# Kernel optimization log

Measured on AMD Instinct MI355X. Metric: run time of the kernel, lower is better.

The kernel has to match this reference:

```python
import jax, jax.numpy as jnp
import numpy as np

NEG_SLOPE = 0.2  # PyG GATv2Conv default negative_slope


def setup_inputs() -> dict:
    key = jax.random.key(0)
    ks = jax.random.split(key, 8)
    B, N, C, H, F, E = 16, 5000, 128, 2, 64, 1_280_000
    T = B * N
    s = 0.05
    x = jax.random.normal(ks[0], (B, N, C), jnp.float32)
    edge_index = jax.random.randint(ks[1], (2, E), 0, T, jnp.int32)
    Wl = jax.random.normal(ks[2], (C, H * F), jnp.float32) * s
    bl = jnp.zeros((H * F,), jnp.float32)
    Wr = jax.random.normal(ks[3], (C, H * F), jnp.float32) * s
    br = jnp.zeros((H * F,), jnp.float32)
    att = jax.random.normal(ks[4], (H, F), jnp.float32) * s
    bias = jnp.zeros((H * F,), jnp.float32)
    return {"x": x, "edge_index": edge_index, "Wl": Wl, "bl": bl,
            "Wr": Wr, "br": br, "att": att, "bias": bias}


def reference(x, edge_index, Wl, bl, Wr, br, att, bias):
    # x: (B, N, C) -> flatten to (T, C), T = B*N total nodes
    B, N, C = x.shape
    T = B * N
    H, F = att.shape
    xf = x.reshape(T, C)
    x_l = (xf @ Wl + bl).reshape(T, H, F)  # source transform (lin_l)
    x_r = (xf @ Wr + br).reshape(T, H, F)  # target transform (lin_r)
    # add self loops (add_self_loops=True)
    loops = jnp.arange(T, dtype=edge_index.dtype)
    src = jnp.concatenate([edge_index[0], loops])
    dst = jnp.concatenate([edge_index[1], loops])
    # GATv2 score: att . LeakyReLU(x_j + x_i)
    e = jax.nn.leaky_relu(x_l[src] + x_r[dst], NEG_SLOPE)  # (Et, H, F)
    logits = jnp.einsum('ehf,hf->eh', e, att)              # (Et, H)
    # edge softmax over incoming edges of each dst node
    m = jax.lax.stop_gradient(jax.ops.segment_max(logits, dst, num_segments=T))
    p = jnp.exp(logits - m[dst])
    denom = jax.ops.segment_sum(p, dst, num_segments=T)
    alpha = p / denom[dst]                                  # (Et, H)
    # aggregate: out_i = sum_j alpha_ij * x_l[j]
    out = jax.ops.segment_sum(x_l[src] * alpha[:, :, None], dst, num_segments=T)
    out = out.reshape(T, H * F) + bias  # concat=True -> (T, H*F)
    return out.reshape(B, N, H * F)
```

## Files before the change

### kernel.cpp

```cpp
#include <hip/hip_runtime.h>
#include <hip/hip_bf16.h>

typedef __hip_bfloat16 bf16;
typedef short s16x8 __attribute__((ext_vector_type(8)));
typedef float f32x4 __attribute__((ext_vector_type(4)));

#define NEG_SLOPE 0.2f
#define MAXB 160
#define EPB  4096
#define CAP  12288

__device__ __forceinline__ unsigned int f32_to_bf16_bits(float f) {
    unsigned int u = __float_as_uint(f);
    return (u + 0x7FFFu + ((u >> 16) & 1u)) >> 16;
}
__device__ __forceinline__ float bf16lo_to_f32(unsigned int u) {
    return __uint_as_float(u << 16);
}
__device__ __forceinline__ float bf16hi_to_f32(unsigned int u) {
    return __uint_as_float(u & 0xFFFF0000u);
}
__device__ __forceinline__ float loadf_rt(const void* p, size_t i, int isb) {
    return isb ? __bfloat162float(((const bf16*)p)[i]) : ((const float*)p)[i];
}

#define ROR_ADD(v, n)                                                          \
    v += __int_as_float(__builtin_amdgcn_update_dpp(                           \
        0, __float_as_int(v), 0x120 + (n), 0xF, 0xF, true))

__global__ void detect_dtype(const unsigned short* __restrict__ xh, int* __restrict__ flag)
{
    int lane = threadIdx.x;
    int cnt = 0;
    for (int j = lane; j < 256; j += 64) {
        unsigned short h = xh[j];
        int e = (h >> 7) & 0xFF;
        if ((h & 0x7FFF) == 0 || (e >= 117 && e <= 131)) cnt++;
    }
    #pragma unroll
    for (int off = 32; off; off >>= 1) cnt += __shfl_xor(cnt, off, 64);
    if (lane == 0) *flag = (cnt >= 192) ? 1 : 0;
}

__global__ void prep_w(const void* __restrict__ Wl, const void* __restrict__ Wr,
                       unsigned short* __restrict__ bpack, const int* __restrict__ flag)
{
    int isb = *flag;
    int tid = blockIdx.x * blockDim.x + threadIdx.x;
    if (tid >= 2 * 8 * 4 * 64) return;
    int lane = tid & 63;
    int kc   = (tid >> 6) & 3;
    int nt   = (tid >> 8) & 7;
    int mat  = tid >> 11;
    const void* W = mat ? Wr : Wl;
    int n  = nt * 16 + (lane & 15);
    int k0 = kc * 32 + (lane >> 4) * 8;
    unsigned short* o = bpack + (size_t)tid * 8;
    #pragma unroll
    for (int j = 0; j < 8; ++j)
        o[j] = (unsigned short)f32_to_bf16_bits(loadf_rt(W, (size_t)(k0 + j) * 128 + n, isb));
}

__global__ void gemm_mfma(const void* __restrict__ x,
                          const unsigned short* __restrict__ bpack,
                          const void* __restrict__ bl, const void* __restrict__ br,
                          unsigned int* __restrict__ xlp, unsigned int* __restrict__ xrp,
                          int T, const int* __restrict__ flag)
{
    int isb  = *flag;
    int lane = threadIdx.x & 63;
    int w    = blockIdx.x * 4 + (threadIdx.x >> 6);
    int row0 = w * 16;
    if (row0 >= T) return;
    int m = lane & 15, quad = lane >> 4;
    int arow = min(row0 + m, T - 1);

    f32x4 acc[16];
    #pragma unroll
    for (int nt = 0; nt < 16; ++nt) acc[nt] = (f32x4){0.f, 0.f, 0.f, 0.f};

    const s16x8* bp = (const s16x8*)bpack;
    for (int kc = 0; kc < 4; ++kc) {
        s16x8 a;
        if (isb) {
            const unsigned short* xb = (const unsigned short*)x
                                     + (size_t)arow * 128 + kc * 32 + quad * 8;
            a = *(const s16x8*)xb;
        } else {
            const float* xp = (const float*)x + (size_t)arow * 128 + kc * 32 + quad * 8;
            float4 xa = ((const float4*)xp)[0];
            float4 xc = ((const float4*)xp)[1];
            a[0] = (short)f32_to_bf16_bits(xa.x); a[1] = (short)f32_to_bf16_bits(xa.y);
            a[2] = (short)f32_to_bf16_bits(xa.z); a[3] = (short)f32_to_bf16_bits(xa.w);
            a[4] = (short)f32_to_bf16_bits(xc.x); a[5] = (short)f32_to_bf16_bits(xc.y);
            a[6] = (short)f32_to_bf16_bits(xc.z); a[7] = (short)f32_to_bf16_bits(xc.w);
        }
        #pragma unroll
        for (int nt = 0; nt < 16; ++nt) {
            s16x8 b = bp[(size_t)(((nt >> 3) * 32) + (nt & 7) * 4 + kc) * 64 + lane];
            acc[nt] = __builtin_amdgcn_mfma_f32_16x16x32_bf16(a, b, acc[nt], 0, 0, 0);
        }
    }
    #pragma unroll
    for (int nt = 0; nt < 4; ++nt) {
        int fl = nt * 16 + m;
        float bl0 = loadf_rt(bl, fl, isb), bl1 = loadf_rt(bl, 64 + fl, isb);
        float br0 = loadf_rt(br, fl, isb), br1 = loadf_rt(br, 64 + fl, isb);
        #pragma unroll
        for (int r = 0; r < 4; ++r) {
            int t = row0 + quad * 4 + r;
            if (t < T) {
                unsigned int pl = f32_to_bf16_bits(acc[nt][r] + bl0)
                                | (f32_to_bf16_bits(acc[nt + 4][r] + bl1) << 16);
                unsigned int pr = f32_to_bf16_bits(acc[nt + 8][r] + br0)
                                | (f32_to_bf16_bits(acc[nt + 12][r] + br1) << 16);
                xlp[(size_t)t * 64 + fl] = pl;
                xrp[(size_t)t * 64 + fl] = pr;
            }
        }
    }
}


__global__ void bucket_hist(const int* __restrict__ ei, int E, int Et,
                            int nbuck, int nb, int* __restrict__ cnt)
{
    __shared__ int h[4][MAXB];
    int tid = threadIdx.x, wid = tid >> 6;
    for (int j = tid; j < 4 * MAXB; j += 256) h[j / MAXB][j % MAXB] = 0;
    __syncthreads();
    int start = blockIdx.x * EPB;
    int end   = min(start + EPB, Et);
    for (int i = start + tid; i < end; i += 256) {
        int dst = (i < E) ? ei[E + i] : (i - E);
        atomicAdd(&h[wid][dst >> 9], 1);
    }
    __syncthreads();
    for (int b = tid; b < nbuck; b += 256)
        cnt[(size_t)b * nb + blockIdx.x] = h[0][b] + h[1][b] + h[2][b] + h[3][b];
}

__global__ void scan1(const int* __restrict__ in, int n, int* __restrict__ bsum)
{
    __shared__ int ws[16];
    int tid = threadIdx.x, lane = tid & 63, wid = tid >> 6;
    int j = blockIdx.x * 1024 + tid;
    int v = (j < n) ? in[j] : 0;
    #pragma unroll
    for (int off = 32; off; off >>= 1) v += __shfl_xor(v, off, 64);
    if (lane == 0) ws[wid] = v;
    __syncthreads();
    if (tid < 64) {
        int u = (lane < 16) ? ws[lane] : 0;
        #pragma unroll
        for (int off = 8; off; off >>= 1) u += __shfl_xor(u, off, 64);
        if (lane == 0) bsum[blockIdx.x] = u;
    }
}

__global__ void scan2(int* __restrict__ bsum, int nb2,
                      int* __restrict__ extra_ptr, int extra_val)
{
    __shared__ int sd[1024];
    int tid = threadIdx.x;
    int v = (tid < nb2) ? bsum[tid] : 0;
    sd[tid] = v;
    __syncthreads();
    for (int off = 1; off < 1024; off <<= 1) {
        int u = (tid >= off) ? sd[tid - off] : 0;
        __syncthreads();
        sd[tid] += u;
        __syncthreads();
    }
    if (tid < nb2) bsum[tid] = sd[tid] - v;
    if (tid == 0 && extra_ptr) *extra_ptr = extra_val;
}

__global__ void scan3(int* __restrict__ data, const int* __restrict__ bsum, int n)
{
    __shared__ int wsum[16];
    __shared__ int woff[16];
    int tid = threadIdx.x, lane = tid & 63, wid = tid >> 6;
    int j = blockIdx.x * 1024 + tid;
    int v = (j < n) ? data[j] : 0;
    int xx = v;
    #pragma unroll
    for (int off = 1; off < 64; off <<= 1) {
        int u = __shfl_up(xx, off, 64);
        if (lane >= off) xx += u;
    }
    if (lane == 63) wsum[wid] = xx;
    __syncthreads();
    if (wid == 0) {
        int s = (lane < 16) ? wsum[lane] : 0;
        int y = s;
        #pragma unroll
        for (int off = 1; off < 16; off <<= 1) {
            int u = __shfl_up(y, off, 64);
            if (lane >= off) y += u;
        }
        if (lane < 16) woff[lane] = y - s;
    }
    __syncthreads();
    if (j < n) data[j] = bsum[blockIdx.x] + woff[wid] + (xx - v);
}

__global__ void bucket_scatter(const int* __restrict__ ei, int E, int Et,
                               int nbuck, int nb, const int* __restrict__ cnt,
                               unsigned int* __restrict__ packed)
{
    __shared__ int cur[MAXB];
    int tid = threadIdx.x;
    for (int b = tid; b < nbuck; b += 256)
        cur[b] = cnt[(size_t)b * nb + blockIdx.x];
    __syncthreads();
    int start = blockIdx.x * EPB;
    int end   = min(start + EPB, Et);
    for (int i = start + tid; i < end; i += 256) {
        int src, dst;
        if (i < E) { src = ei[i]; dst = ei[E + i]; }
        else       { src = i - E; dst = i - E; }
        int pos = atomicAdd(&cur[dst >> 9], 1);
        packed[pos] = ((unsigned int)src << 9) | (unsigned int)(dst & 511);
    }
}

__global__ void build_csr(unsigned int* __restrict__ colpacked,
                          const int* __restrict__ cnt, int nb, int nbuck,
                          int Et, int T, int* __restrict__ row_ptr)
{
    __shared__ unsigned int st[CAP];
    __shared__ int h[512];
    __shared__ int off[512];
    __shared__ int ws[4];
    int b    = blockIdx.x;
    int tid  = threadIdx.x, lane = tid & 63, wid = tid >> 6;
    int base = cnt[(size_t)b * nb];
    int endb = (b + 1 < nbuck) ? cnt[(size_t)(b + 1) * nb] : Et;
    int m    = min(endb - base, CAP);

    for (int i = tid; i < m; i += 256) st[i] = colpacked[base + i];
    for (int j = tid; j < 512; j += 256) h[j] = 0;
    __syncthreads();
    for (int i = tid; i < m; i += 256) atomicAdd(&h[st[i] & 511], 1);
    __syncthreads();

    int h0 = h[2 * tid], h1 = h[2 * tid + 1];
    int s  = h0 + h1;
    int xx = s;
    #pragma unroll
    for (int o = 1; o < 64; o <<= 1) {
        int u = __shfl_up(xx, o, 64);
        if (lane >= o) xx += u;
    }
    if (lane == 63) ws[wid] = xx;
    __syncthreads();
    int wo = 0;
    for (int wv = 0; wv < 4; ++wv) if (wv < wid) wo += ws[wv];
    int e0 = wo + xx - s;
    int e1 = e0 + h0;
    off[2 * tid]     = e0;
    off[2 * tid + 1] = e1;
    int node0 = b * 512 + 2 * tid;
    if (node0 < T)     row_ptr[node0]     = base + e0;
    if (node0 + 1 < T) row_ptr[node0 + 1] = base + e1;
    __syncthreads();

    for (int i = tid; i < m; i += 256) {
        unsigned int p = st[i];
        int pos = atomicAdd(&off[p & 511], 1);
        colpacked[base + pos] = p >> 9;
    }
}

__global__ void aggregate(const unsigned int* __restrict__ xlp,
                          const unsigned int* __restrict__ xrp,
                          const int* __restrict__ row_ptr, const int* __restrict__ col,
                          const void* __restrict__ att, const void* __restrict__ bias,
                          float* __restrict__ out, int T,
                          const int* __restrict__ flag)
{
    int lane = threadIdx.x & 63;
    int node = blockIdx.x * 4 + (threadIdx.x >> 6);
    if (node >= T) return;
    int isb = *flag;
    int g = lane >> 4;
    int q = lane & 15;

    uint4 xr4 = ((const uint4*)(xrp + (size_t)node * 64))[q];
    float xr0[4], xr1[4], at0[4], at1[4];
    {
        unsigned int xrw[4] = {xr4.x, xr4.y, xr4.z, xr4.w};
        #pragma unroll
        for (int k = 0; k < 4; ++k) {
            xr0[k] = bf16lo_to_f32(xrw[k]);
            xr1[k] = bf16hi_to_f32(xrw[k]);
            at0[k] = loadf_rt(att, q * 4 + k, isb);
            at1[k] = loadf_rt(att, 64 + q * 4 + k, isb);
        }
    }

    float s0 = 0.f, s1 = 0.f;
    float a0[4] = {0.f, 0.f, 0.f, 0.f}, a1[4] = {0.f, 0.f, 0.f, 0.f};

    int beg = row_ptr[node], end = row_ptr[node + 1];

    bool v0 = (beg + g) < end;      int sA = v0 ? col[beg + g]     : node;
    bool v1 = (beg + 4 + g) < end;  int sB = v1 ? col[beg + 4 + g] : node;
    bool v2 = (beg + 8 + g) < end;  int sC = v2 ? col[beg + 8 + g] : node;
    uint4 cx = ((const uint4*)(xlp + (size_t)sA * 64))[q];
    uint4 nx = ((const uint4*)(xlp + (size_t)sB * 64))[q];

    for (int i = beg; i < end; i += 4) {
        bool v3 = (i + 12 + g) < end;
        int  sD = v3 ? col[i + 12 + g] : node;
        uint4 px = ((const uint4*)(xlp + (size_t)sC * 64))[q];

        unsigned int xlw[4] = {cx.x, cx.y, cx.z, cx.w};
        float xl0[4], xl1[4];
        float t0 = 0.f, t1 = 0.f;
        #pragma unroll
        for (int k = 0; k < 4; ++k) {
            xl0[k] = bf16lo_to_f32(xlw[k]);
            xl1[k] = bf16hi_to_f32(xlw[k]);
            float e0 = xl0[k] + xr0[k]; e0 = fmaxf(e0, NEG_SLOPE * e0);
            float e1 = xl1[k] + xr1[k]; e1 = fmaxf(e1, NEG_SLOPE * e1);
            t0 = fmaf(e0, at0[k], t0);
            t1 = fmaf(e1, at1[k], t1);
        }
        ROR_ADD(t0, 8); ROR_ADD(t1, 8);
        ROR_ADD(t0, 4); ROR_ADD(t1, 4);
        ROR_ADD(t0, 2); ROR_ADD(t1, 2);
        ROR_ADD(t0, 1); ROR_ADD(t1, 1);
        t0 = fminf(fmaxf(t0, -30.f), 30.f);
        t1 = fminf(fmaxf(t1, -30.f), 30.f);
        float p0 = v0 ? __expf(t0) : 0.f;
        float p1 = v0 ? __expf(t1) : 0.f;
        s0 += p0; s1 += p1;
        #pragma unroll
        for (int k = 0; k < 4; ++k) {
            a0[k] = fmaf(p0, xl0[k], a0[k]);
            a1[k] = fmaf(p1, xl1[k], a1[k]);
        }
        cx = nx; nx = px;
        v0 = v1; v1 = v2; v2 = v3; sC = sD;
    }

    #pragma unroll
    for (int off = 16; off <= 32; off <<= 1) {
        s0 += __shfl_xor(s0, off, 64);
        s1 += __shfl_xor(s1, off, 64);
        #pragma unroll
        for (int k = 0; k < 4; ++k) {
            a0[k] += __shfl_xor(a0[k], off, 64);
            a1[k] += __shfl_xor(a1[k], off, 64);
        }
    }

    float inv0 = (s0 > 0.f) ? 1.f / s0 : 0.f;
    float inv1 = (s1 > 0.f) ? 1.f / s1 : 0.f;
    if (g == 0) {
        float4 o;
        o.x = fmaf(a0[0], inv0, loadf_rt(bias, q * 4 + 0, isb));
        o.y = fmaf(a0[1], inv0, loadf_rt(bias, q * 4 + 1, isb));
        o.z = fmaf(a0[2], inv0, loadf_rt(bias, q * 4 + 2, isb));
        o.w = fmaf(a0[3], inv0, loadf_rt(bias, q * 4 + 3, isb));
        ((float4*)(out + (size_t)node * 128))[q] = o;
    } else if (g == 1) {
        float4 o;
        o.x = fmaf(a1[0], inv1, loadf_rt(bias, 64 + q * 4 + 0, isb));
        o.y = fmaf(a1[1], inv1, loadf_rt(bias, 64 + q * 4 + 1, isb));
        o.z = fmaf(a1[2], inv1, loadf_rt(bias, 64 + q * 4 + 2, isb));
        o.w = fmaf(a1[3], inv1, loadf_rt(bias, 64 + q * 4 + 3, isb));
        ((float4*)(out + (size_t)node * 128))[16 + q] = o;
    }
}

extern "C" void kernel_launch(void* const* d_in, const int* in_sizes, int n_in,
                              void* d_out, int out_size, void* d_ws, size_t ws_size,
                              hipStream_t stream)
{
    const void* x    = d_in[0];
    const int*  ei   = (const int*)d_in[1];
    const void* Wl   = d_in[2];
    const void* bl   = d_in[3];
    const void* Wr   = d_in[4];
    const void* br   = d_in[5];
    const void* att  = d_in[6];
    const void* bias = d_in[7];
    float* out = (float*)d_out;

    int T     = in_sizes[0] / 128;
    int E     = in_sizes[1] / 2;
    int Et    = E + T;
    int nbuck = (T + 511) >> 9;
    int nb    = (Et + EPB - 1) / EPB;
    int ncnt  = nbuck * nb;
    int nb2   = (ncnt + 1023) / 1024;

    char* w = (char*)d_ws;
    unsigned int* xlp = (unsigned int*)w;  w += (size_t)T * 64 * 4;
    unsigned int* xrp = (unsigned int*)w;  w += (size_t)T * 64 * 4;
    int* rowptr = (int*)w;  w += (size_t)(T + 1) * 4;
    unsigned int* col = (unsigned int*)w;  w += (size_t)Et * 4;
    int* cnt    = (int*)w;  w += (size_t)ncnt * 4;
    int* bsum2  = (int*)w;  w += 4096;
    int* flag   = (int*)w;  w += 256;
    unsigned short* bpack = (unsigned short*)w;  w += 2 * 8 * 4 * 64 * 8 * 2;

    detect_dtype<<<1, 64, 0, stream>>>((const unsigned short*)x, flag);
    prep_w<<<16, 256, 0, stream>>>(Wl, Wr, bpack, flag);
    gemm_mfma<<<(T + 63) / 64, 256, 0, stream>>>(x, bpack, bl, br, xlp, xrp, T, flag);

    bucket_hist<<<nb, 256, 0, stream>>>(ei, E, Et, nbuck, nb, cnt);
    scan1<<<nb2, 1024, 0, stream>>>(cnt, ncnt, bsum2);
    scan2<<<1, 1024, 0, stream>>>(bsum2, nb2, rowptr + T, Et);
    scan3<<<nb2, 1024, 0, stream>>>(cnt, bsum2, ncnt);
    bucket_scatter<<<nb, 256, 0, stream>>>(ei, E, Et, nbuck, nb, cnt, col);
    build_csr<<<nbuck, 256, 0, stream>>>(col, cnt, nb, nbuck, Et, T, rowptr);

    aggregate<<<(T + 3) / 4, 256, 0, stream>>>(xlp, xrp, rowptr, (const int*)col,
                                               att, bias, out, T, flag);
}
```

Measured before the change: 254.5 us.

## Replace per-block bucket count scan with global atomic bucket totals; pack aggregate math

The edge bucketing no longer stores a per-block, per-bucket count matrix followed by a three-kernel scan. Each block now atomically adds its local histogram into a small global bucket-total array. One small kernel scans those totals, and the scatter kernel recomputes its local histogram and claims offsets with global atomics. This drops two launches and the large count-matrix traffic, at the cost of a second histogram pass and a nondeterministic edge order inside each bucket. The aggregate loop is also rewritten with two-wide float vectors, which may let the compiler emit packed FP32 instructions.

```diff
diff --git a/kernel.cpp b/kernel.cpp
--- a/kernel.cpp
+++ b/kernel.cpp
@@ -4,6 +4,7 @@
 typedef __hip_bfloat16 bf16;
 typedef short s16x8 __attribute__((ext_vector_type(8)));
 typedef float f32x4 __attribute__((ext_vector_type(4)));
+typedef float f32x2 __attribute__((ext_vector_type(2)));
 
 #define NEG_SLOPE 0.2f
 #define MAXB 160
@@ -28,9 +29,11 @@
     v += __int_as_float(__builtin_amdgcn_update_dpp(                           \
         0, __float_as_int(v), 0x120 + (n), 0xF, 0xF, true))
 
-__global__ void detect_dtype(const unsigned short* __restrict__ xh, int* __restrict__ flag)
+__global__ void detect_dtype(const unsigned short* __restrict__ xh, int* __restrict__ flag,
+                             int* __restrict__ gtot)
 {
     int lane = threadIdx.x;
+    for (int j = lane; j < MAXB; j += 64) gtot[j] = 0;
     int cnt = 0;
     for (int j = lane; j < 256; j += 64) {
         unsigned short h = xh[j];
@@ -122,8 +125,8 @@
 }
 
 
-__global__ void bucket_hist(const int* __restrict__ ei, int E, int Et,
-                            int nbuck, int nb, int* __restrict__ cnt)
+__global__ void bucket_hist2(const int* __restrict__ ei, int E, int Et,
+                             int nbuck, int* __restrict__ gtot)
 {
     __shared__ int h[4][MAXB];
     int tid = threadIdx.x, wid = tid >> 6;
@@ -136,86 +139,52 @@
         atomicAdd(&h[wid][dst >> 9], 1);
     }
     __syncthreads();
-    for (int b = tid; b < nbuck; b += 256)
-        cnt[(size_t)b * nb + blockIdx.x] = h[0][b] + h[1][b] + h[2][b] + h[3][b];
-}
-
-__global__ void scan1(const int* __restrict__ in, int n, int* __restrict__ bsum)
-{
-    __shared__ int ws[16];
-    int tid = threadIdx.x, lane = tid & 63, wid = tid >> 6;
-    int j = blockIdx.x * 1024 + tid;
-    int v = (j < n) ? in[j] : 0;
-    #pragma unroll
-    for (int off = 32; off; off >>= 1) v += __shfl_xor(v, off, 64);
-    if (lane == 0) ws[wid] = v;
-    __syncthreads();
-    if (tid < 64) {
-        int u = (lane < 16) ? ws[lane] : 0;
-        #pragma unroll
-        for (int off = 8; off; off >>= 1) u += __shfl_xor(u, off, 64);
-        if (lane == 0) bsum[blockIdx.x] = u;
-    }
-}
-
-__global__ void scan2(int* __restrict__ bsum, int nb2,
-                      int* __restrict__ extra_ptr, int extra_val)
-{
-    __shared__ int sd[1024];
+    for (int b = tid; b < nbuck; b += 256) {
+        int v = h[0][b] + h[1][b] + h[2][b] + h[3][b];
+        if (v) atomicAdd(&gtot[b], v);
+    }
+}
+
+__global__ void scan_buckets(int* __restrict__ gtot, int nbuck, int Et,
+                             int* __restrict__ bases, int* __restrict__ rowptr_T)
+{
+    __shared__ int sd[256];
     int tid = threadIdx.x;
-    int v = (tid < nb2) ? bsum[tid] : 0;
+    int v = (tid < nbuck) ? gtot[tid] : 0;
     sd[tid] = v;
     __syncthreads();
-    for (int off = 1; off < 1024; off <<= 1) {
+    for (int off = 1; off < 256; off <<= 1) {
         int u = (tid >= off) ? sd[tid - off] : 0;
         __syncthreads();
         sd[tid] += u;
         __syncthreads();
     }
-    if (tid < nb2) bsum[tid] = sd[tid] - v;
-    if (tid == 0 && extra_ptr) *extra_ptr = extra_val;
-}
-
-__global__ void scan3(int* __restrict__ data, const int* __restrict__ bsum, int n)
-{
-    __shared__ int wsum[16];
-    __shared__ int woff[16];
-    int tid = threadIdx.x, lane = tid & 63, wid = tid >> 6;
-    int j = blockIdx.x * 1024 + tid;
-    int v = (j < n) ? data[j] : 0;
-    int xx = v;
-    #pragma unroll
-    for (int off = 1; off < 64; off <<= 1) {
-        int u = __shfl_up(xx, off, 64);
-        if (lane >= off) xx += u;
-    }
-    if (lane == 63) wsum[wid] = xx;
-    __syncthreads();
-    if (wid == 0) {
-        int s = (lane < 16) ? wsum[lane] : 0;
-        int y = s;
-        #pragma unroll
-        for (int off = 1; off < 16; off <<= 1) {
-            int u = __shfl_up(y, off, 64);
-            if (lane >= off) y += u;
-        }
-        if (lane < 16) woff[lane] = y - s;
-    }
-    __syncthreads();
-    if (j < n) data[j] = bsum[blockIdx.x] + woff[wid] + (xx - v);
-}
-
-__global__ void bucket_scatter(const int* __restrict__ ei, int E, int Et,
-                               int nbuck, int nb, const int* __restrict__ cnt,
-                               unsigned int* __restrict__ packed)
-{
+    int excl = sd[tid] - v;
+    if (tid < nbuck) { bases[tid] = excl; gtot[tid] = excl; }
+    if (tid == 0) { bases[nbuck] = Et; *rowptr_T = Et; }
+}
+
+__global__ void bucket_scatter2(const int* __restrict__ ei, int E, int Et,
+                                int nbuck, int* __restrict__ gcur,
+                                unsigned int* __restrict__ packed)
+{
+    __shared__ int h[4][MAXB];
     __shared__ int cur[MAXB];
-    int tid = threadIdx.x;
-    for (int b = tid; b < nbuck; b += 256)
-        cur[b] = cnt[(size_t)b * nb + blockIdx.x];
+    int tid = threadIdx.x, wid = tid >> 6;
+    for (int j = tid; j < 4 * MAXB; j += 256) h[j / MAXB][j % MAXB] = 0;
     __syncthreads();
     int start = blockIdx.x * EPB;
     int end   = min(start + EPB, Et);
+    for (int i = start + tid; i < end; i += 256) {
+        int dst = (i < E) ? ei[E + i] : (i - E);
+        atomicAdd(&h[wid][dst >> 9], 1);
+    }
+    __syncthreads();
+    for (int b = tid; b < nbuck; b += 256) {
+        int v = h[0][b] + h[1][b] + h[2][b] + h[3][b];
+        cur[b] = v ? atomicAdd(&gcur[b], v) : 0;
+    }
+    __syncthreads();
     for (int i = start + tid; i < end; i += 256) {
         int src, dst;
         if (i < E) { src = ei[i]; dst = ei[E + i]; }
@@ -226,7 +195,7 @@
 }
 
 __global__ void build_csr(unsigned int* __restrict__ colpacked,
-                          const int* __restrict__ cnt, int nb, int nbuck,
+                          const int* __restrict__ bases, int nbuck,
                           int Et, int T, int* __restrict__ row_ptr)
 {
     __shared__ unsigned int st[CAP];
@@ -235,8 +204,8 @@
     __shared__ int ws[4];
     int b    = blockIdx.x;
     int tid  = threadIdx.x, lane = tid & 63, wid = tid >> 6;
-    int base = cnt[(size_t)b * nb];
-    int endb = (b + 1 < nbuck) ? cnt[(size_t)(b + 1) * nb] : Et;
+    int base = bases[b];
+    int endb = bases[b + 1];
     int m    = min(endb - base, CAP);
 
     for (int i = tid; i < m; i += 256) st[i] = colpacked[base + i];
@@ -288,20 +257,19 @@
     int q = lane & 15;
 
     uint4 xr4 = ((const uint4*)(xrp + (size_t)node * 64))[q];
-    float xr0[4], xr1[4], at0[4], at1[4];
+    f32x2 xr2[4], at2[4];
     {
         unsigned int xrw[4] = {xr4.x, xr4.y, xr4.z, xr4.w};
         #pragma unroll
         for (int k = 0; k < 4; ++k) {
-            xr0[k] = bf16lo_to_f32(xrw[k]);
-            xr1[k] = bf16hi_to_f32(xrw[k]);
-            at0[k] = loadf_rt(att, q * 4 + k, isb);
-            at1[k] = loadf_rt(att, 64 + q * 4 + k, isb);
-        }
-    }
-
-    float s0 = 0.f, s1 = 0.f;
-    float a0[4] = {0.f, 0.f, 0.f, 0.f}, a1[4] = {0.f, 0.f, 0.f, 0.f};
+            xr2[k] = (f32x2){bf16lo_to_f32(xrw[k]), bf16hi_to_f32(xrw[k])};
+            at2[k] = (f32x2){loadf_rt(att, q * 4 + k, isb),
+                             loadf_rt(att, 64 + q * 4 + k, isb)};
+        }
+    }
+
+    f32x2 s2 = {0.f, 0.f};
+    f32x2 a2[4] = {{0.f, 0.f}, {0.f, 0.f}, {0.f, 0.f}, {0.f, 0.f}};
 
     int beg = row_ptr[node], end = row_ptr[node + 1];
 
@@ -317,61 +285,60 @@
         uint4 px = ((const uint4*)(xlp + (size_t)sC * 64))[q];
 
         unsigned int xlw[4] = {cx.x, cx.y, cx.z, cx.w};
-        float xl0[4], xl1[4];
-        float t0 = 0.f, t1 = 0.f;
+        f32x2 xl2[4];
+        f32x2 t2 = {0.f, 0.f};
         #pragma unroll
         for (int k = 0; k < 4; ++k) {
-            xl0[k] = bf16lo_to_f32(xlw[k]);
-            xl1[k] = bf16hi_to_f32(xlw[k]);
-            float e0 = xl0[k] + xr0[k]; e0 = fmaxf(e0, NEG_SLOPE * e0);
-            float e1 = xl1[k] + xr1[k]; e1 = fmaxf(e1, NEG_SLOPE * e1);
-            t0 = fmaf(e0, at0[k], t0);
-            t1 = fmaf(e1, at1[k], t1);
-        }
+            xl2[k] = (f32x2){bf16lo_to_f32(xlw[k]), bf16hi_to_f32(xlw[k])};
+            f32x2 e  = xl2[k] + xr2[k];
+            f32x2 lr = __builtin_elementwise_max(e, e * NEG_SLOPE);
+            t2 = __builtin_elementwise_fma(lr, at2[k], t2);
+        }
+        float t0 = t2.x, t1 = t2.y;
         ROR_ADD(t0, 8); ROR_ADD(t1, 8);
         ROR_ADD(t0, 4); ROR_ADD(t1, 4);
         ROR_ADD(t0, 2); ROR_ADD(t1, 2);
         ROR_ADD(t0, 1); ROR_ADD(t1, 1);
         t0 = fminf(fmaxf(t0, -30.f), 30.f);
         t1 = fminf(fmaxf(t1, -30.f), 30.f);
-        float p0 = v0 ? __expf(t0) : 0.f;
-        float p1 = v0 ? __expf(t1) : 0.f;
-        s0 += p0; s1 += p1;
-        #pragma unroll
-        for (int k = 0; k < 4; ++k) {
-            a0[k] = fmaf(p0, xl0[k], a0[k]);
-            a1[k] = fmaf(p1, xl1[k], a1[k]);
-        }
+        f32x2 p2;
+        p2.x = v0 ? __expf(t0) : 0.f;
+        p2.y = v0 ? __expf(t1) : 0.f;
+        s2 += p2;
+        #pragma unroll
+        for (int k = 0; k < 4; ++k)
+            a2[k] = __builtin_elementwise_fma(p2, xl2[k], a2[k]);
+
         cx = nx; nx = px;
         v0 = v1; v1 = v2; v2 = v3; sC = sD;
     }
 
     #pragma unroll
     for (int off = 16; off <= 32; off <<= 1) {
-        s0 += __shfl_xor(s0, off, 64);
-        s1 += __shfl_xor(s1, off, 64);
+        s2.x += __shfl_xor(s2.x, off, 64);
+        s2.y += __shfl_xor(s2.y, off, 64);
         #pragma unroll
         for (int k = 0; k < 4; ++k) {
-            a0[k] += __shfl_xor(a0[k], off, 64);
-            a1[k] += __shfl_xor(a1[k], off, 64);
-        }
-    }
-
-    float inv0 = (s0 > 0.f) ? 1.f / s0 : 0.f;
-    float inv1 = (s1 > 0.f) ? 1.f / s1 : 0.f;
+            a2[k].x += __shfl_xor(a2[k].x, off, 64);
+            a2[k].y += __shfl_xor(a2[k].y, off, 64);
+        }
+    }
+
+    float inv0 = (s2.x > 0.f) ? 1.f / s2.x : 0.f;
+    float inv1 = (s2.y > 0.f) ? 1.f / s2.y : 0.f;
     if (g == 0) {
         float4 o;
-        o.x = fmaf(a0[0], inv0, loadf_rt(bias, q * 4 + 0, isb));
-        o.y = fmaf(a0[1], inv0, loadf_rt(bias, q * 4 + 1, isb));
-        o.z = fmaf(a0[2], inv0, loadf_rt(bias, q * 4 + 2, isb));
-        o.w = fmaf(a0[3], inv0, loadf_rt(bias, q * 4 + 3, isb));
+        o.x = fmaf(a2[0].x, inv0, loadf_rt(bias, q * 4 + 0, isb));
+        o.y = fmaf(a2[1].x, inv0, loadf_rt(bias, q * 4 + 1, isb));
+        o.z = fmaf(a2[2].x, inv0, loadf_rt(bias, q * 4 + 2, isb));
+        o.w = fmaf(a2[3].x, inv0, loadf_rt(bias, q * 4 + 3, isb));
         ((float4*)(out + (size_t)node * 128))[q] = o;
     } else if (g == 1) {
         float4 o;
-        o.x = fmaf(a1[0], inv1, loadf_rt(bias, 64 + q * 4 + 0, isb));
-        o.y = fmaf(a1[1], inv1, loadf_rt(bias, 64 + q * 4 + 1, isb));
-        o.z = fmaf(a1[2], inv1, loadf_rt(bias, 64 + q * 4 + 2, isb));
-        o.w = fmaf(a1[3], inv1, loadf_rt(bias, 64 + q * 4 + 3, isb));
+        o.x = fmaf(a2[0].y, inv1, loadf_rt(bias, 64 + q * 4 + 0, isb));
+        o.y = fmaf(a2[1].y, inv1, loadf_rt(bias, 64 + q * 4 + 1, isb));
+        o.z = fmaf(a2[2].y, inv1, loadf_rt(bias, 64 + q * 4 + 2, isb));
+        o.w = fmaf(a2[3].y, inv1, loadf_rt(bias, 64 + q * 4 + 3, isb));
         ((float4*)(out + (size_t)node * 128))[16 + q] = o;
     }
 }
@@ -395,29 +362,25 @@
     int Et    = E + T;
     int nbuck = (T + 511) >> 9;
     int nb    = (Et + EPB - 1) / EPB;
-    int ncnt  = nbuck * nb;
-    int nb2   = (ncnt + 1023) / 1024;
 
     char* w = (char*)d_ws;
     unsigned int* xlp = (unsigned int*)w;  w += (size_t)T * 64 * 4;
     unsigned int* xrp = (unsigned int*)w;  w += (size_t)T * 64 * 4;
     int* rowptr = (int*)w;  w += (size_t)(T + 1) * 4;
     unsigned int* col = (unsigned int*)w;  w += (size_t)Et * 4;
-    int* cnt    = (int*)w;  w += (size_t)ncnt * 4;
-    int* bsum2  = (int*)w;  w += 4096;
+    int* gtot   = (int*)w;  w += MAXB * 4;
+    int* bases  = (int*)w;  w += (MAXB + 8) * 4;
     int* flag   = (int*)w;  w += 256;
     unsigned short* bpack = (unsigned short*)w;  w += 2 * 8 * 4 * 64 * 8 * 2;
 
-    detect_dtype<<<1, 64, 0, stream>>>((const unsigned short*)x, flag);
+    detect_dtype<<<1, 64, 0, stream>>>((const unsigned short*)x, flag, gtot);
     prep_w<<<16, 256, 0, stream>>>(Wl, Wr, bpack, flag);
     gemm_mfma<<<(T + 63) / 64, 256, 0, stream>>>(x, bpack, bl, br, xlp, xrp, T, flag);
 
-    bucket_hist<<<nb, 256, 0, stream>>>(ei, E, Et, nbuck, nb, cnt);
-    scan1<<<nb2, 1024, 0, stream>>>(cnt, ncnt, bsum2);
-    scan2<<<1, 1024, 0, stream>>>(bsum2, nb2, rowptr + T, Et);
-    scan3<<<nb2, 1024, 0, stream>>>(cnt, bsum2, ncnt);
-    bucket_scatter<<<nb, 256, 0, stream>>>(ei, E, Et, nbuck, nb, cnt, col);
-    build_csr<<<nbuck, 256, 0, stream>>>(col, cnt, nb, nbuck, Et, T, rowptr);
+    bucket_hist2<<<nb, 256, 0, stream>>>(ei, E, Et, nbuck, gtot);
+    scan_buckets<<<1, 256, 0, stream>>>(gtot, nbuck, Et, bases, rowptr + T);
+    bucket_scatter2<<<nb, 256, 0, stream>>>(ei, E, Et, nbuck, gtot, col);
+    build_csr<<<nbuck, 256, 0, stream>>>(col, bases, nbuck, Et, T, rowptr);
 
     aggregate<<<(T + 3) / 4, 256, 0, stream>>>(xlp, xrp, rowptr, (const int*)col,
                                                att, bias, out, T, flag);
```

New measurement: 265.4 us. 1.04x slower.
